# Kernel optimization log

Hardware: AMD Instinct MI355X
Metric: run time of the kernel (lower is better)

Reference implementation:

```python
import jax, jax.numpy as jnp
import numpy as np
import math

H = 2
NC, NPR = 100000, 50000
IN, HID, OUT = 128, 128, 16
E1, E2 = 300000, 300000
D = HID // H


def _segment_softmax(scores, seg, num_segments):
    m = jax.ops.segment_max(scores, seg, num_segments=num_segments)
    m = jax.lax.stop_gradient(jnp.where(jnp.isfinite(m), m, 0.0))
    e = jnp.exp(scores - m[seg])
    s = jax.ops.segment_sum(e, seg, num_segments=num_segments)
    return e / (s[seg] + 1e-16)


def _hgt_layer(xc, xp, ecp_s, ecp_d, epc_s, epc_d, prm):
    (wc, bc, wp, bp, acp, mcp, pcp, apc, mpc, ppc,
     owc, obc, owp, obp, sc, sp) = prm
    Nc, Np = xc.shape[0], xp.shape[0]

    def kqv(x, w, b):
        t = x @ w + b
        k, q, v = jnp.split(t, 3, axis=1)
        d = k.shape[1] // H
        return k.reshape(-1, H, d), q.reshape(-1, H, d), v.reshape(-1, H, d)

    kc, qc, vc = kqv(xc, wc, bc)
    kp, qp, vp = kqv(xp, wp, bp)
    d = kc.shape[-1]
    # relation-specific transforms applied to source-node keys/values (a_rel / m_rel)
    k_cp = jnp.einsum('nhd,hde->nhe', kc, acp)
    v_cp = jnp.einsum('nhd,hde->nhe', vc, mcp)
    k_pc = jnp.einsum('nhd,hde->nhe', kp, apc)
    v_pc = jnp.einsum('nhd,hde->nhe', vp, mpc)
    # merged destination index space: customers [0,Nc), products [Nc,Nc+Np)
    q_all = jnp.concatenate([qc, qp], axis=0)
    kj = jnp.concatenate([k_cp[ecp_s], k_pc[epc_s]], axis=0)  # [E,H,D] per-edge gather
    vj = jnp.concatenate([v_cp[ecp_s], v_pc[epc_s]], axis=0)
    dst = jnp.concatenate([ecp_d + Nc, epc_d], axis=0)
    prel = jnp.concatenate([jnp.broadcast_to(pcp, (ecp_s.shape[0], H)),
                            jnp.broadcast_to(ppc, (epc_s.shape[0], H))], axis=0)
    alpha = (q_all[dst] * kj).sum(-1) * prel / math.sqrt(d)  # [E,H]
    alpha = _segment_softmax(alpha, dst, Nc + Np)  # softmax over all incoming edges per dst node
    out = jax.ops.segment_sum(vj * alpha[..., None], dst, num_segments=Nc + Np)
    out = out.reshape(Nc + Np, H * d)

    def mix(o, x, ow, ob, s):
        o = jax.nn.gelu(o, approximate=False) @ ow + ob
        g = jax.nn.sigmoid(s)
        return g * o + (1.0 - g) * x

    return mix(out[:Nc], xc, owc, obc, sc), mix(out[Nc:], xp, owp, obp, sp)


def setup_inputs():
    key = jax.random.key(0)
    ks = list(jax.random.split(key, 64))
    it = iter(range(64))

    def nrm(shape, scale):
        return jax.random.normal(ks[next(it)], shape, dtype=jnp.float32) * scale

    inp = {}
    inp['xc'] = nrm((NC, IN), 1.0)
    inp['xp'] = nrm((NPR, IN), 1.0)
    for l in (1, 2):
        fin = IN if l == 1 else HID
        inp[f'w{l}c'] = nrm((fin, 3 * HID), 0.08)
        inp[f'b{l}c'] = jnp.zeros((3 * HID,), jnp.float32)
        inp[f'w{l}p'] = nrm((fin, 3 * HID), 0.08)
        inp[f'b{l}p'] = jnp.zeros((3 * HID,), jnp.float32)
        for et in ('cp', 'pc'):
            inp[f'a{l}{et}'] = nrm((H, D, D), 0.125)
            inp[f'm{l}{et}'] = nrm((H, D, D), 0.125)
            inp[f'p{l}{et}'] = jnp.ones((H,), jnp.float32)
        inp[f'ow{l}c'] = nrm((HID, HID), 0.08)
        inp[f'ob{l}c'] = jnp.zeros((HID,), jnp.float32)
        inp[f'ow{l}p'] = nrm((HID, HID), 0.08)
        inp[f'ob{l}p'] = jnp.zeros((HID,), jnp.float32)
        inp[f's{l}c'] = jnp.ones((1,), jnp.float32)
        inp[f's{l}p'] = jnp.ones((1,), jnp.float32)
    inp['wl'] = nrm((HID, OUT), 0.08)
    inp['bl'] = jnp.zeros((OUT,), jnp.float32)
    inp['ecp_s'] = jax.random.randint(ks[next(it)], (E1,), 0, NC, dtype=jnp.int32)
    inp['ecp_d'] = jax.random.randint(ks[next(it)], (E1,), 0, NPR, dtype=jnp.int32)
    inp['epc_s'] = jax.random.randint(ks[next(it)], (E2,), 0, NPR, dtype=jnp.int32)
    inp['epc_d'] = jax.random.randint(ks[next(it)], (E2,), 0, NC, dtype=jnp.int32)
    return inp


def reference(xc, xp, w1c, b1c, w1p, b1p, a1cp, m1cp, p1cp, a1pc, m1pc, p1pc, ow1c, ob1c, ow1p, ob1p, s1c, s1p, w2c, b2c, w2p, b2p, a2cp, m2cp, p2cp, a2pc, m2pc, p2pc, ow2c, ob2c, ow2p, ob2p, s2c, s2p, wl, bl, ecp_s, ecp_d, epc_s, epc_d):
    oc, op = _hgt_layer(xc, xp, ecp_s, ecp_d, epc_s, epc_d,
                        (w1c, b1c, w1p, b1p, a1cp, m1cp, p1cp, a1pc, m1pc, p1pc, ow1c, ob1c, ow1p, ob1p, s1c, s1p))
    oc, op = jax.nn.relu(oc), jax.nn.relu(op)
    oc, op = _hgt_layer(oc, op, ecp_s, ecp_d, epc_s, epc_d,
                        (w2c, b2c, w2p, b2p, a2cp, m2cp, p2cp, a2pc, m2pc, p2pc, ow2c, ob2c, ow2p, ob2p, s2c, s2p))
    return oc @ wl + bl
```

## Files before the change

### kernel.cpp

```cpp
#include <hip/hip_runtime.h>

typedef __attribute__((ext_vector_type(8))) short s16x8;
typedef __attribute__((ext_vector_type(4))) float f32x4;

constexpr int kNC = 100000;
constexpr int kNP = 50000;
constexpr int kNT = kNC + kNP;
constexpr int kE1 = 300000;
constexpr int kE2 = 300000;
constexpr int kCAP = 32;

__device__ __forceinline__ float geluf(float x) {
    return 0.5f * x * (1.0f + erff(x * 0.7071067811865475f));
}
__device__ __forceinline__ unsigned short f2bf(float f) {
    unsigned int u = __float_as_uint(f);
    u += 0x7fffu + ((u >> 16) & 1u);
    return (unsigned short)(u >> 16);
}
__device__ __forceinline__ float bf2f(unsigned short s) {
    return __uint_as_float(((unsigned int)s) << 16);
}

__global__ __launch_bounds__(256) void cvt_bf16(
    const float* __restrict__ in, unsigned short* __restrict__ out, int n8)
{
    int i = blockIdx.x * 256 + threadIdx.x;
    if (i >= n8) return;
    float4 a = *(const float4*)(in + (size_t)i * 8);
    float4 b = *(const float4*)(in + (size_t)i * 8 + 4);
    ushort4 o0 = { f2bf(a.x), f2bf(a.y), f2bf(a.z), f2bf(a.w) };
    ushort4 o1 = { f2bf(b.x), f2bf(b.y), f2bf(b.z), f2bf(b.w) };
    *(ushort4*)(out + (size_t)i * 8) = o0;
    *(ushort4*)(out + (size_t)i * 8 + 4) = o1;
}

__global__ __launch_bounds__(128) void cvt_wT(
    const float* __restrict__ src, int ldb, unsigned short* __restrict__ dst)
{
    int c = blockIdx.x;
    int r = threadIdx.x;
    dst[(size_t)c * 128 + r] = f2bf(src[(size_t)r * ldb + c]);
}

__global__ void fold_k(const float* __restrict__ w, const float* __restrict__ b,
                       const float* __restrict__ ar, const float* __restrict__ mr,
                       unsigned short* __restrict__ wt, float* __restrict__ beff) {
    int col = blockIdx.x;
    int i = threadIdx.x;
    float acc, bacc;
    if (col >= 128 && col < 256) {
        acc = w[i * 384 + col];
        bacc = b[col];
    } else {
        const float* rel = (col < 128) ? ar : mr;
        int base = (col < 128) ? 0 : 256;
        int c = col - base;
        int h = c >> 6, j = c & 63;
        acc = 0.0f; bacc = 0.0f;
        for (int d = 0; d < 64; ++d) {
            float rv = rel[(h * 64 + d) * 64 + j];
            acc  = fmaf(w[i * 384 + base + h * 64 + d], rv, acc);
            bacc = fmaf(b[base + h * 64 + d], rv, bacc);
        }
    }
    wt[(size_t)col * 128 + i] = f2bf(acc);
    if (i == 0) beff[col] = bacc;
}

struct Job {
    const unsigned short* WT;
    const float* bias;
    const unsigned short* A;
    const unsigned short* Xres;
    const float* sgate;
    void* out;
    int M;
    int omap;
    int roleOff;
};

template<int PRO, int EPI, int RELU, int FINAL>
__global__ __launch_bounds__(256) void gemm64(
    Job j0, Job j1, Job j2, Job j3, Job j4, Job j5,
    const unsigned short* __restrict__ wlt, const float* __restrict__ blv)
{
    Job J;
    switch (blockIdx.y) {
        case 0: J = j0; break;
        case 1: J = j1; break;
        case 2: J = j2; break;
        case 3: J = j3; break;
        case 4: J = j4; break;
        default: J = j5; break;
    }
    const int row0 = blockIdx.x * 64;
    const int M = J.M;
    if (row0 >= M) return;

    constexpr int NSM = FINAL ? (64 * 132) : (64 * 36 + 128 * 36);
    __shared__ unsigned short sm[NSM];
    unsigned short* As = sm;
    unsigned short* Bs = sm + 64 * 36;

    const int t = threadIdx.x;
    const int lane = t & 63;
    const int w = t >> 6;
    const int l15 = lane & 15, l4 = lane >> 4;

    f32x4 acc[8];
    #pragma unroll
    for (int n = 0; n < 8; ++n) {
        float bv = J.bias[n * 16 + l15];
        acc[n] = f32x4{bv, bv, bv, bv};
    }

    union FR { uint2 u[2]; s16x8 v; };

    for (int kc = 0; kc < 4; ++kc) {
        const int k0 = kc * 32;
        ushort4 a_[2];
        #pragma unroll
        for (int i = 0; i < 2; ++i) {
            int idx = i * 256 + t;
            int r = idx >> 3, kq = idx & 7;
            int gr = row0 + r;
            ushort4 rv = {0, 0, 0, 0};
            if (gr < M) rv = *(const ushort4*)(J.A + (size_t)gr * 128 + k0 + kq * 4);
            if (PRO) {
                rv.x = f2bf(geluf(bf2f(rv.x)));
                rv.y = f2bf(geluf(bf2f(rv.y)));
                rv.z = f2bf(geluf(bf2f(rv.z)));
                rv.w = f2bf(geluf(bf2f(rv.w)));
            }
            a_[i] = rv;
        }
        ushort4 b_[4];
        #pragma unroll
        for (int i = 0; i < 4; ++i) {
            int idx = i * 256 + t;
            int c = idx >> 3, kq = idx & 7;
            b_[i] = *(const ushort4*)(J.WT + (size_t)c * 128 + k0 + kq * 4);
        }
        if (kc) __syncthreads();
        #pragma unroll
        for (int i = 0; i < 2; ++i) {
            int idx = i * 256 + t;
            int r = idx >> 3, kq = idx & 7;
            *(ushort4*)&As[r * 36 + kq * 4] = a_[i];
        }
        #pragma unroll
        for (int i = 0; i < 4; ++i) {
            int idx = i * 256 + t;
            int c = idx >> 3, kq = idx & 7;
            *(ushort4*)&Bs[c * 36 + kq * 4] = b_[i];
        }
        __syncthreads();

        FR af;
        {
            const unsigned short* p = &As[(w * 16 + l15) * 36 + l4 * 4];
            af.u[0] = *(const uint2*)p;
            af.u[1] = *(const uint2*)(p + 16);
        }
        #pragma unroll
        for (int n = 0; n < 8; ++n) {
            const unsigned short* p = &Bs[(n * 16 + l15) * 36 + l4 * 4];
            FR bfr;
            bfr.u[0] = *(const uint2*)p;
            bfr.u[1] = *(const uint2*)(p + 16);
            acc[n] = __builtin_amdgcn_mfma_f32_16x16x32_bf16(af.v, bfr.v, acc[n], 0, 0, 0);
        }
    }

    float g = 0.f, omg = 0.f;
    if (EPI == 1) { g = 1.0f / (1.0f + expf(-J.sgate[0])); omg = 1.0f - g; }

    if (FINAL) __syncthreads();

    #pragma unroll
    for (int r = 0; r < 4; ++r) {
        int lr = w * 16 + l4 * 4 + r;
        int gr = row0 + lr;
        bool ok = gr < M;
        #pragma unroll
        for (int n = 0; n < 8; ++n) {
            float v = acc[n][r];
            if (EPI == 1) {
                float xv = ok ? bf2f(J.Xres[(size_t)gr * 128 + n * 16 + l15]) : 0.f;
                v = g * v + omg * xv;
                if (RELU) v = fmaxf(v, 0.0f);
            }
            if (FINAL) {
                sm[lr * 132 + n * 16 + l15] = f2bf(v);
            } else if (ok) {
                unsigned short hv = f2bf(v);
                int c = n * 16 + l15;
                if (J.omap)
                    ((unsigned short*)J.out)[(size_t)gr * 256 + ((c >> 1) << 2) + (c & 1) + J.roleOff] = hv;
                else
                    ((unsigned short*)J.out)[(size_t)gr * 128 + c] = hv;
            }
        }
    }

    if (FINAL) {
        f32x4 facc;
        float bv = blv[l15];
        facc = f32x4{bv, bv, bv, bv};
        #pragma unroll
        for (int kc2 = 0; kc2 < 4; ++kc2) {
            FR bfr, afr;
            #pragma unroll
            for (int h = 0; h < 2; ++h) {
                bfr.u[h] = *(const uint2*)&wlt[(size_t)l15 * 128 + kc2 * 32 + h * 16 + l4 * 4];
                afr.u[h] = *(const uint2*)&sm[(w * 16 + l15) * 132 + kc2 * 32 + h * 16 + l4 * 4];
            }
            facc = __builtin_amdgcn_mfma_f32_16x16x32_bf16(afr.v, bfr.v, facc, 0, 0, 0);
        }
        #pragma unroll
        for (int r = 0; r < 4; ++r) {
            int gr = row0 + w * 16 + l4 * 4 + r;
            if (gr < M) ((float*)J.out)[(size_t)gr * 16 + l15] = facc[r];
        }
    }
}

__global__ __launch_bounds__(256) void build_bucket(
    const int* __restrict__ src, const int* __restrict__ dst, int E,
    int* __restrict__ cnt, int* __restrict__ bucket)
{
    int e = blockIdx.x * 256 + threadIdx.x;
    if (e >= E) return;
    int d = dst[e];
    int slot = atomicAdd(&cnt[d], 1);
    if (slot < kCAP) bucket[(size_t)d * kCAP + slot] = src[e];
}

__global__ __launch_bounds__(256) void fused_attn2(
    int nA, const int* __restrict__ cntA, const int* __restrict__ bucketA,
    const unsigned short* __restrict__ kvA, unsigned short* __restrict__ qoA,
    const float* __restrict__ prelA,
    int nB, const int* __restrict__ cntB, const int* __restrict__ bucketB,
    const unsigned short* __restrict__ kvB, unsigned short* __restrict__ qoB,
    const float* __restrict__ prelB)
{
    int wid = (blockIdx.x * 256 + threadIdx.x) >> 6;
    int lane = threadIdx.x & 63;
    const int* cnt; const int* bucket; const unsigned short* kvs;
    unsigned short* qo; const float* prel;
    if (wid < nA) {
        cnt = cntA; bucket = bucketA; kvs = kvA; qo = qoA; prel = prelA;
    } else {
        wid -= nA;
        if (wid >= nB) return;
        cnt = cntB; bucket = bucketB; kvs = kvB; qo = qoB; prel = prelB;
    }
    int deg = cnt[wid];
    if (deg > kCAP) deg = kCAP;
    int mys = (lane < deg) ? bucket[(size_t)wid * kCAP + lane] : 0;
    unsigned int qv = *(const unsigned int*)(qo + (size_t)wid * 128 + lane * 2);
    float qx = bf2f((unsigned short)qv), qy = bf2f((unsigned short)(qv >> 16));
    float ph = prel[lane >> 5] * 0.125f;

    float ss = 0.f, o0 = 0.f, o1 = 0.f;
    int i = 0;
    for (; i + 2 <= deg; i += 2) {
        int s0 = __shfl(mys, i);
        int s1 = __shfl(mys, i + 1);
        uint2 kv0 = *(const uint2*)(kvs + (size_t)s0 * 256 + lane * 4);
        uint2 kv1 = *(const uint2*)(kvs + (size_t)s1 * 256 + lane * 4);
        float p0 = qx * bf2f((unsigned short)kv0.x) + qy * bf2f((unsigned short)(kv0.x >> 16));
        float p1 = qx * bf2f((unsigned short)kv1.x) + qy * bf2f((unsigned short)(kv1.x >> 16));
        p0 += __shfl_xor(p0, 1);  p1 += __shfl_xor(p1, 1);
        p0 += __shfl_xor(p0, 2);  p1 += __shfl_xor(p1, 2);
        p0 += __shfl_xor(p0, 4);  p1 += __shfl_xor(p1, 4);
        p0 += __shfl_xor(p0, 8);  p1 += __shfl_xor(p1, 8);
        p0 += __shfl_xor(p0, 16); p1 += __shfl_xor(p1, 16);
        float w0 = __expf(p0 * ph);
        float w1 = __expf(p1 * ph);
        ss += w0;
        o0 = fmaf(w0, bf2f((unsigned short)kv0.y), o0);
        o1 = fmaf(w0, bf2f((unsigned short)(kv0.y >> 16)), o1);
        ss += w1;
        o0 = fmaf(w1, bf2f((unsigned short)kv1.y), o0);
        o1 = fmaf(w1, bf2f((unsigned short)(kv1.y >> 16)), o1);
    }
    if (i < deg) {
        int s = __shfl(mys, i);
        uint2 kv = *(const uint2*)(kvs + (size_t)s * 256 + lane * 4);
        float p = qx * bf2f((unsigned short)kv.x) + qy * bf2f((unsigned short)(kv.x >> 16));
        p += __shfl_xor(p, 1);
        p += __shfl_xor(p, 2);
        p += __shfl_xor(p, 4);
        p += __shfl_xor(p, 8);
        p += __shfl_xor(p, 16);
        float wgt = __expf(p * ph);
        ss += wgt;
        o0 = fmaf(wgt, bf2f((unsigned short)kv.y), o0);
        o1 = fmaf(wgt, bf2f((unsigned short)(kv.y >> 16)), o1);
    }
    float rr = 1.0f / (ss + 1e-16f);
    unsigned int ov = (unsigned)f2bf(o0 * rr) | ((unsigned)f2bf(o1 * rr) << 16);
    *(unsigned int*)(qo + (size_t)wid * 128 + lane * 2) = ov;
}

extern "C" void kernel_launch(void* const* d_in, const int* in_sizes, int n_in,
                              void* d_out, int out_size, void* d_ws, size_t ws_size,
                              hipStream_t stream)
{
    const float* xc  = (const float*)d_in[0];
    const float* xp  = (const float*)d_in[1];
    const float* w1c = (const float*)d_in[2];
    const float* b1c = (const float*)d_in[3];
    const float* w1p = (const float*)d_in[4];
    const float* b1p = (const float*)d_in[5];
    const float* a1cp= (const float*)d_in[6];
    const float* m1cp= (const float*)d_in[7];
    const float* p1cp= (const float*)d_in[8];
    const float* a1pc= (const float*)d_in[9];
    const float* m1pc= (const float*)d_in[10];
    const float* p1pc= (const float*)d_in[11];
    const float* ow1c= (const float*)d_in[12];
    const float* ob1c= (const float*)d_in[13];
    const float* ow1p= (const float*)d_in[14];
    const float* ob1p= (const float*)d_in[15];
    const float* s1c = (const float*)d_in[16];
    const float* s1p = (const float*)d_in[17];
    const float* w2c = (const float*)d_in[18];
    const float* b2c = (const float*)d_in[19];
    const float* w2p = (const float*)d_in[20];
    const float* b2p = (const float*)d_in[21];
    const float* a2pc= (const float*)d_in[25];
    const float* m2pc= (const float*)d_in[26];
    const float* p2pc= (const float*)d_in[27];
    const float* ow2c= (const float*)d_in[28];
    const float* ob2c= (const float*)d_in[29];
    const float* s2c = (const float*)d_in[32];
    const float* wl  = (const float*)d_in[34];
    const float* bl  = (const float*)d_in[35];
    const int* ecp_s = (const int*)d_in[36];
    const int* ecp_d = (const int*)d_in[37];
    const int* epc_s = (const int*)d_in[38];
    const int* epc_d = (const int*)d_in[39];
    float* outF = (float*)d_out;
    (void)in_sizes; (void)n_in; (void)out_size; (void)ws_size;

    char* ws = (char*)d_ws;
    size_t off = 0;
    auto take = [&](size_t bytes) { char* p = ws + off; off += (bytes + 255) & ~(size_t)255; return p; };
    char* R0 = take((size_t)kNC * 256 * 2);
    unsigned short* kvC = (unsigned short*)R0;
    unsigned short* hcb = (unsigned short*)R0;
    unsigned short* kvP = (unsigned short*)take((size_t)kNP * 256 * 2);
    unsigned short* qAll = (unsigned short*)take((size_t)kNT * 128 * 2);
    unsigned short* qC = qAll;
    unsigned short* qP = qAll + (size_t)kNC * 128;
    unsigned short* hp = (unsigned short*)take((size_t)kNP * 128 * 2);
    int* cntP = (int*)take((size_t)kNP * 4);
    int* cntC = (int*)take((size_t)kNC * 4);
    int* bucketP = (int*)take((size_t)kNP * kCAP * 4);
    int* bucketC = (int*)take((size_t)kNC * kCAP * 4);
    unsigned short* wecT = (unsigned short*)take((size_t)384 * 128 * 2);
    unsigned short* wepT = (unsigned short*)take((size_t)384 * 128 * 2);
    unsigned short* ow1cT= (unsigned short*)take((size_t)128 * 128 * 2);
    unsigned short* ow1pT= (unsigned short*)take((size_t)128 * 128 * 2);
    unsigned short* ow2cT= (unsigned short*)take((size_t)128 * 128 * 2);
    unsigned short* w2cqT= (unsigned short*)take((size_t)128 * 128 * 2);
    unsigned short* wlT  = (unsigned short*)take((size_t)16 * 128 * 2);
    float* bec = (float*)take((size_t)384 * 4);
    float* bep = (float*)take((size_t)384 * 4);
    unsigned short* xcb = (unsigned short*)take((size_t)kNC * 128 * 2);
    unsigned short* xpb = (unsigned short*)take((size_t)kNP * 128 * 2);

    auto cdiv = [](int a, int b) { return (a + b - 1) / b; };
    dim3 blk(256);
    const int gx = cdiv(kNC, 64);
    const float* nf = nullptr;
    const unsigned short* nu = nullptr;

    hipMemsetAsync(cntP, 0, (size_t)kNP * 4, stream);
    hipMemsetAsync(cntC, 0, (size_t)kNC * 4, stream);
    hipLaunchKernelGGL(build_bucket, dim3(cdiv(kE1, 256)), blk, 0, stream, ecp_s, ecp_d, kE1, cntP, bucketP);
    hipLaunchKernelGGL(build_bucket, dim3(cdiv(kE2, 256)), blk, 0, stream, epc_s, epc_d, kE2, cntC, bucketC);

    hipLaunchKernelGGL(cvt_bf16, dim3(cdiv(kNC * 16, 256)), blk, 0, stream, xc, xcb, kNC * 16);
    hipLaunchKernelGGL(cvt_bf16, dim3(cdiv(kNP * 16, 256)), blk, 0, stream, xp, xpb, kNP * 16);
    hipLaunchKernelGGL(cvt_wT, dim3(128), dim3(128), 0, stream, ow1c, 128, ow1cT);
    hipLaunchKernelGGL(cvt_wT, dim3(128), dim3(128), 0, stream, ow1p, 128, ow1pT);
    hipLaunchKernelGGL(cvt_wT, dim3(128), dim3(128), 0, stream, ow2c, 128, ow2cT);
    hipLaunchKernelGGL(cvt_wT, dim3(128), dim3(128), 0, stream, w2c + 128, 384, w2cqT);
    hipLaunchKernelGGL(cvt_wT, dim3(16),  dim3(128), 0, stream, wl, 16, wlT);

    hipLaunchKernelGGL(fold_k, dim3(384), dim3(128), 0, stream, w1c, b1c, a1cp, m1cp, wecT, bec);
    hipLaunchKernelGGL(fold_k, dim3(384), dim3(128), 0, stream, w1p, b1p, a1pc, m1pc, wepT, bep);

    Job jkC = { wecT + 0,       bec + 0,   xcb, nu, nf, (void*)kvC, kNC, 1, 0 };
    Job jqC = { wecT + 128*128, bec + 128, xcb, nu, nf, (void*)qC,  kNC, 0, 0 };
    Job jvC = { wecT + 256*128, bec + 256, xcb, nu, nf, (void*)kvC, kNC, 1, 2 };
    Job jkP = { wepT + 0,       bep + 0,   xpb, nu, nf, (void*)kvP, kNP, 1, 0 };
    Job jqP = { wepT + 128*128, bep + 128, xpb, nu, nf, (void*)qP,  kNP, 0, 0 };
    Job jvP = { wepT + 256*128, bep + 256, xpb, nu, nf, (void*)kvP, kNP, 1, 2 };
    hipLaunchKernelGGL((gemm64<0,0,0,0>), dim3(gx, 6), blk, 0, stream,
                       jkC, jqC, jvC, jkP, jqP, jvP, nu, nf);

    hipLaunchKernelGGL(fused_attn2, dim3(cdiv(kNP + kNC, 4)), blk, 0, stream,
                       kNP, cntP, bucketP, kvC, qP, p1cp,
                       kNC, cntC, bucketC, kvP, qC, p1pc);

    Job jmC = { ow1cT, ob1c, qC, xcb, s1c, (void*)hcb, kNC, 0, 0 };
    Job jmP = { ow1pT, ob1p, qP, xpb, s1p, (void*)hp,  kNP, 0, 0 };
    hipLaunchKernelGGL((gemm64<1,1,1,0>), dim3(gx, 2), blk, 0, stream,
                       jmC, jmP, jmC, jmC, jmC, jmC, nu, nf);

    hipLaunchKernelGGL(fold_k, dim3(384), dim3(128), 0, stream, w2p, b2p, a2pc, m2pc, wepT, bep);
    Job jk2 = { wepT + 0,       bep + 0,   hp,  nu, nf, (void*)kvP, kNP, 1, 0 };
    Job jv2 = { wepT + 256*128, bep + 256, hp,  nu, nf, (void*)kvP, kNP, 1, 2 };
    Job jq2 = { w2cqT,          b2c + 128, hcb, nu, nf, (void*)qC,  kNC, 0, 0 };
    hipLaunchKernelGGL((gemm64<0,0,0,0>), dim3(gx, 3), blk, 0, stream,
                       jk2, jv2, jq2, jk2, jk2, jk2, nu, nf);

    hipLaunchKernelGGL(fused_attn2, dim3(cdiv(kNC, 4)), blk, 0, stream,
                       kNC, cntC, bucketC, kvP, qC, p2pc,
                       0, cntC, bucketC, kvP, qC, p2pc);

    Job jf = { ow2cT, ob2c, qC, hcb, s2c, (void*)outF, kNC, 0, 0 };
    hipLaunchKernelGGL((gemm64<1,1,0,1>), dim3(gx, 1), blk, 0, stream,
                       jf, jf, jf, jf, jf, jf, wlT, bl);
}
```

Measured before the change: 376.4 us.

## Process two edges per wavefront with 16-byte K/V gathers in attention

```diff
diff --git a/kernel.cpp b/kernel.cpp
--- a/kernel.cpp
+++ b/kernel.cpp
@@ -21,6 +21,8 @@
 __device__ __forceinline__ float bf2f(unsigned short s) {
     return __uint_as_float(((unsigned int)s) << 16);
 }
+__device__ __forceinline__ float bfLo(unsigned int w) { return __uint_as_float(w << 16); }
+__device__ __forceinline__ float bfHi(unsigned int w) { return __uint_as_float(w & 0xffff0000u); }
 
 __global__ __launch_bounds__(256) void cvt_bf16(
     const float* __restrict__ in, unsigned short* __restrict__ out, int n8)
@@ -197,7 +199,7 @@
                 unsigned short hv = f2bf(v);
                 int c = n * 16 + l15;
                 if (J.omap)
-                    ((unsigned short*)J.out)[(size_t)gr * 256 + ((c >> 1) << 2) + (c & 1) + J.roleOff] = hv;
+                    ((unsigned short*)J.out)[(size_t)gr * 256 + ((c >> 2) << 3) + (c & 3) + J.roleOff] = hv;
                 else
                     ((unsigned short*)J.out)[(size_t)gr * 128 + c] = hv;
             }
@@ -258,51 +260,44 @@
     }
     int deg = cnt[wid];
     if (deg > kCAP) deg = kCAP;
+    const int l31 = lane & 31;
     int mys = (lane < deg) ? bucket[(size_t)wid * kCAP + lane] : 0;
-    unsigned int qv = *(const unsigned int*)(qo + (size_t)wid * 128 + lane * 2);
-    float qx = bf2f((unsigned short)qv), qy = bf2f((unsigned short)(qv >> 16));
-    float ph = prel[lane >> 5] * 0.125f;
-
-    float ss = 0.f, o0 = 0.f, o1 = 0.f;
-    int i = 0;
-    for (; i + 2 <= deg; i += 2) {
-        int s0 = __shfl(mys, i);
-        int s1 = __shfl(mys, i + 1);
-        uint2 kv0 = *(const uint2*)(kvs + (size_t)s0 * 256 + lane * 4);
-        uint2 kv1 = *(const uint2*)(kvs + (size_t)s1 * 256 + lane * 4);
-        float p0 = qx * bf2f((unsigned short)kv0.x) + qy * bf2f((unsigned short)(kv0.x >> 16));
-        float p1 = qx * bf2f((unsigned short)kv1.x) + qy * bf2f((unsigned short)(kv1.x >> 16));
-        p0 += __shfl_xor(p0, 1);  p1 += __shfl_xor(p1, 1);
-        p0 += __shfl_xor(p0, 2);  p1 += __shfl_xor(p1, 2);
-        p0 += __shfl_xor(p0, 4);  p1 += __shfl_xor(p1, 4);
-        p0 += __shfl_xor(p0, 8);  p1 += __shfl_xor(p1, 8);
-        p0 += __shfl_xor(p0, 16); p1 += __shfl_xor(p1, 16);
-        float w0 = __expf(p0 * ph);
-        float w1 = __expf(p1 * ph);
-        ss += w0;
-        o0 = fmaf(w0, bf2f((unsigned short)kv0.y), o0);
-        o1 = fmaf(w0, bf2f((unsigned short)(kv0.y >> 16)), o1);
-        ss += w1;
-        o0 = fmaf(w1, bf2f((unsigned short)kv1.y), o0);
-        o1 = fmaf(w1, bf2f((unsigned short)(kv1.y >> 16)), o1);
-    }
-    if (i < deg) {
-        int s = __shfl(mys, i);
-        uint2 kv = *(const uint2*)(kvs + (size_t)s * 256 + lane * 4);
-        float p = qx * bf2f((unsigned short)kv.x) + qy * bf2f((unsigned short)(kv.x >> 16));
+    uint2 qv = *(const uint2*)(qo + (size_t)wid * 128 + l31 * 4);
+    float q0 = bfLo(qv.x), q1 = bfHi(qv.x), q2 = bfLo(qv.y), q3 = bfHi(qv.y);
+    float ph = prel[l31 >> 4] * 0.125f;
+
+    float ss = 0.f, o0 = 0.f, o1 = 0.f, o2 = 0.f, o3 = 0.f;
+    const int half = lane >> 5;
+    const int nIt = (deg + 1) >> 1;
+    for (int i = 0; i < nIt; ++i) {
+        int idx = 2 * i + half;
+        bool valid = idx < deg;
+        int s = __shfl(mys, valid ? idx : 0);
+        uint4 kv = *(const uint4*)(kvs + (size_t)s * 256 + l31 * 8);
+        float p = q0 * bfLo(kv.x) + q1 * bfHi(kv.x) + q2 * bfLo(kv.y) + q3 * bfHi(kv.y);
         p += __shfl_xor(p, 1);
         p += __shfl_xor(p, 2);
         p += __shfl_xor(p, 4);
         p += __shfl_xor(p, 8);
-        p += __shfl_xor(p, 16);
-        float wgt = __expf(p * ph);
+        float wgt = valid ? __expf(p * ph) : 0.f;
         ss += wgt;
-        o0 = fmaf(wgt, bf2f((unsigned short)kv.y), o0);
-        o1 = fmaf(wgt, bf2f((unsigned short)(kv.y >> 16)), o1);
-    }
+        o0 = fmaf(wgt, bfLo(kv.z), o0);
+        o1 = fmaf(wgt, bfHi(kv.z), o1);
+        o2 = fmaf(wgt, bfLo(kv.w), o2);
+        o3 = fmaf(wgt, bfHi(kv.w), o3);
+    }
+    ss += __shfl_xor(ss, 32);
+    o0 += __shfl_xor(o0, 32);
+    o1 += __shfl_xor(o1, 32);
+    o2 += __shfl_xor(o2, 32);
+    o3 += __shfl_xor(o3, 32);
     float rr = 1.0f / (ss + 1e-16f);
-    unsigned int ov = (unsigned)f2bf(o0 * rr) | ((unsigned)f2bf(o1 * rr) << 16);
-    *(unsigned int*)(qo + (size_t)wid * 128 + lane * 2) = ov;
+    if (lane < 32) {
+        uint2 ov;
+        ov.x = (unsigned)f2bf(o0 * rr) | ((unsigned)f2bf(o1 * rr) << 16);
+        ov.y = (unsigned)f2bf(o2 * rr) | ((unsigned)f2bf(o3 * rr) << 16);
+        *(uint2*)(qo + (size_t)wid * 128 + l31 * 4) = ov;
+    }
 }
 
 extern "C" void kernel_launch(void* const* d_in, const int* in_sizes, int n_in,
@@ -397,10 +392,10 @@
 
     Job jkC = { wecT + 0,       bec + 0,   xcb, nu, nf, (void*)kvC, kNC, 1, 0 };
     Job jqC = { wecT + 128*128, bec + 128, xcb, nu, nf, (void*)qC,  kNC, 0, 0 };
-    Job jvC = { wecT + 256*128, bec + 256, xcb, nu, nf, (void*)kvC, kNC, 1, 2 };
+    Job jvC = { wecT + 256*128, bec + 256, xcb, nu, nf, (void*)kvC, kNC, 1, 4 };
     Job jkP = { wepT + 0,       bep + 0,   xpb, nu, nf, (void*)kvP, kNP, 1, 0 };
     Job jqP = { wepT + 128*128, bep + 128, xpb, nu, nf, (void*)qP,  kNP, 0, 0 };
-    Job jvP = { wepT + 256*128, bep + 256, xpb, nu, nf, (void*)kvP, kNP, 1, 2 };
+    Job jvP = { wepT + 256*128, bep + 256, xpb, nu, nf, (void*)kvP, kNP, 1, 4 };
     hipLaunchKernelGGL((gemm64<0,0,0,0>), dim3(gx, 6), blk, 0, stream,
                        jkC, jqC, jvC, jkP, jqP, jvP, nu, nf);
 
@@ -415,7 +410,7 @@
 
     hipLaunchKernelGGL(fold_k, dim3(384), dim3(128), 0, stream, w2p, b2p, a2pc, m2pc, wepT, bep);
     Job jk2 = { wepT + 0,       bep + 0,   hp,  nu, nf, (void*)kvP, kNP, 1, 0 };
-    Job jv2 = { wepT + 256*128, bep + 256, hp,  nu, nf, (void*)kvP, kNP, 1, 2 };
+    Job jv2 = { wepT + 256*128, bep + 256, hp,  nu, nf, (void*)kvP, kNP, 1, 4 };
     Job jq2 = { w2cqT,          b2c + 128, hcb, nu, nf, (void*)qC,  kNC, 0, 0 };
     hipLaunchKernelGGL((gemm64<0,0,0,0>), dim3(gx, 3), blk, 0, stream,
                        jk2, jv2, jq2, jk2, jk2, jk2, nu, nf);
```

Result: faster. 367.8 us (-2.3%).
